# Kernel tuning notes

Hardware: AMD Instinct MI355X
Metric: run time of the kernel (lower is better)

Reference implementation:

```python
import jax, jax.numpy as jnp
import numpy as np

D = 256
H = 256
B = 128
T = 512


def _init_cell(key, input_size, hidden_size):
    K = 1.0 / np.sqrt(hidden_size)
    k1, k2, k3, k4 = jax.random.split(key, 4)
    u = lambda k, shape: jax.random.uniform(k, shape, jnp.float32, -K, K)
    return (u(k1, (3 * hidden_size, input_size)),
            u(k2, (3 * hidden_size, hidden_size)),
            u(k3, (3 * hidden_size,)),
            u(k4, (3 * hidden_size,)))


def setup_inputs() -> dict:
    key = jax.random.key(0)
    kx, kf, kb = jax.random.split(key, 3)
    x = jax.random.normal(kx, (B, T, D), dtype=jnp.float32)
    w_ih_fw, w_hh_fw, b_ih_fw, b_hh_fw = _init_cell(kf, D, H)
    w_ih_bw, w_hh_bw, b_ih_bw, b_hh_bw = _init_cell(kb, D, H)
    return {
        "x": x,
        "w_ih_fw": w_ih_fw, "w_hh_fw": w_hh_fw, "b_ih_fw": b_ih_fw, "b_hh_fw": b_hh_fw,
        "w_ih_bw": w_ih_bw, "w_hh_bw": w_hh_bw, "b_ih_bw": b_ih_bw, "b_hh_bw": b_hh_bw,
    }


def _gru_scan(x_tbd, w_ih, w_hh, b_ih, b_hh):
    # x_tbd: [T, B, D]; returns outputs [T, B, H] and final h [B, H]
    h0 = jnp.zeros((x_tbd.shape[1], H), dtype=x_tbd.dtype)

    def step(h, x_t):
        xT = x_t @ w_ih.T + b_ih          # [B, 3H]
        hT = h @ w_hh.T + b_hh            # [B, 3H]
        s = jax.nn.sigmoid(xT + hT)
        r = s[:, :H]
        z = s[:, H:2 * H]
        n = jnp.tanh(xT[:, 2 * H:] + r * hT[:, 2 * H:])
        h_new = (1.0 - z) * n + z * h
        return h_new, h_new

    h_last, outs = jax.lax.scan(step, h0, x_tbd)
    return outs, h_last


def reference(x, w_ih_fw, w_hh_fw, b_ih_fw, b_hh_fw,
              w_ih_bw, w_hh_bw, b_ih_bw, b_hh_bw):
    x_tbd = jnp.swapaxes(x, 0, 1)                         # [T, B, D]
    outs_fw, h_fw = _gru_scan(x_tbd, w_ih_fw, w_hh_fw, b_ih_fw, b_hh_fw)
    outs_bw_rev, h_bw = _gru_scan(x_tbd[::-1], w_ih_bw, w_hh_bw, b_ih_bw, b_hh_bw)
    outs_bw = outs_bw_rev[::-1]
    outputs = jnp.concatenate([outs_fw, outs_bw], axis=-1)  # [T, B, 2H]
    outputs = jnp.swapaxes(outputs, 0, 1)                   # [B, T, 2H]
    return outputs, h_fw, h_bw
```

## Files before the change

kernel.cpp:

```cpp
#include <hip/hip_runtime.h>
#include <stdint.h>
#include <stddef.h>

#define T_ 512
#define B_ 128
#define D_ 256
#define H_ 256
#define NR 768
#define OUT_MAIN 33554432ull
#define XT_STRIDE 12288
#define HB 280

typedef __attribute__((ext_vector_type(4))) float f32x4;
typedef __attribute__((ext_vector_type(8))) short s16x8;

__device__ __forceinline__ unsigned short f2bf(float f) {
    union { float f; uint32_t u; } v; v.f = f;
    return (unsigned short)((v.u + 0x7FFFu + ((v.u >> 16) & 1u)) >> 16);
}
__device__ __forceinline__ float bf2f(unsigned short h) {
    union { uint32_t u; float f; } v; v.u = ((uint32_t)h) << 16;
    return v.f;
}
__device__ __forceinline__ float sigm(float x) {
    return __builtin_amdgcn_rcpf(1.f + __expf(-x));
}
__device__ __forceinline__ float tanh_(float x) {
    float e = __expf(2.f * x);
    return 1.f - 2.f * __builtin_amdgcn_rcpf(e + 1.f);
}
__device__ __forceinline__ s16x8 pack8(const float* f) {
    union { s16x8 v; unsigned short u[8]; } p;
#pragma unroll
    for (int i = 0; i < 8; ++i) p.u[i] = f2bf(f[i]);
    return p.v;
}

__global__ void k_convert(const float* __restrict__ wf, const float* __restrict__ wb,
                          unsigned short* __restrict__ dst) {
    int i = blockIdx.x * blockDim.x + threadIdx.x;
    const int n = NR * D_;
    if (i < n) dst[i] = f2bf(wf[i]);
    else if (i < 2 * n) dst[i] = f2bf(wb[i - n]);
}

__global__ __launch_bounds__(512, 2) void k_xgemm(
    const float* __restrict__ x, const unsigned short* __restrict__ wbf,
    const float* __restrict__ bih_f, const float* __restrict__ bhh_f,
    const float* __restrict__ bih_b, const float* __restrict__ bhh_b,
    unsigned short* __restrict__ XT)
{
    __shared__ __align__(16) unsigned short lds_a[64 * 72];
    const int tid = threadIdx.x;
    const int lane = tid & 63, wn = tid >> 6;
    const int t = blockIdx.x;
    const int dir = blockIdx.y >> 1, mh = blockIdx.y & 1;

    f32x4 acc[4][6];
#pragma unroll
    for (int m = 0; m < 4; ++m)
#pragma unroll
        for (int n = 0; n < 6; ++n) acc[m][n] = (f32x4){0.f, 0.f, 0.f, 0.f};

    for (int kb = 0; kb < 4; ++kb) {
        if (kb) __syncthreads();
        {
            int row = tid >> 3, seg = tid & 7;
            const float* src = x + ((size_t)(mh * 64 + row) * T_ + t) * D_ + kb * 64 + seg * 8;
            float fv[8];
            *(f32x4*)&fv[0] = *(const f32x4*)(src);
            *(f32x4*)&fv[4] = *(const f32x4*)(src + 4);
            *(s16x8*)&lds_a[row * 72 + seg * 8] = pack8(fv);
        }
        __syncthreads();
#pragma unroll
        for (int kt = 0; kt < 2; ++kt) {
            s16x8 av[4];
#pragma unroll
            for (int mt = 0; mt < 4; ++mt) {
                int r = mt * 16 + (lane & 15);
                av[mt] = *(const s16x8*)&lds_a[r * 72 + kt * 32 + (lane >> 4) * 8];
            }
#pragma unroll
            for (int nt = 0; nt < 6; ++nt) {
                int c = dir * NR + wn * 96 + nt * 16 + (lane & 15);
                s16x8 bv = *(const s16x8*)(wbf + (size_t)c * D_ + kb * 64 + kt * 32 + (lane >> 4) * 8);
#pragma unroll
                for (int mt = 0; mt < 4; ++mt)
                    acc[mt][nt] = __builtin_amdgcn_mfma_f32_16x16x32_bf16(av[mt], bv, acc[mt][nt], 0, 0, 0);
            }
        }
    }
    const float* bih = dir ? bih_b : bih_f;
    const float* bhh = dir ? bhh_b : bhh_f;
#pragma unroll
    for (int nt = 0; nt < 6; ++nt) {
        const int cw = wn * 96 + nt * 16 + (lane & 15);
        const int gate = cw >> 8, j = cw & 255;
        const int jt = (j >> 4) & 1;
        const int rtid = (j >> 5) * 64 + (((lane >> 4)) << 4) + (j & 15);
        float bias = bih[cw] + (cw < 512 ? bhh[cw] : 0.f);
#pragma unroll
        for (int mt = 0; mt < 4; ++mt) {
#pragma unroll
            for (int q = 0; q < 4; ++q) {
                int rr = mh * 64 + mt * 16 + (lane >> 4) * 4 + q;
                int bgrp = rr >> 4;
                int v = (jt * 4 + q) * 3 + gate;
                XT[((size_t)(dir * 8 + bgrp) * T_ + t) * XT_STRIDE + (size_t)rtid * 24 + v]
                    = f2bf(acc[mt][nt][q] + bias);
            }
        }
    }
}

template<int P>
__device__ __forceinline__ void gru_step(
    int s, int dir, int b0, int tid, int lane, int wid,
    const unsigned short* __restrict__ XTw, float* __restrict__ out,
    unsigned short* hb, const s16x8 (&fB)[6][8], float bhn0, float bhn1,
    s16x8 (&CUR)[3], s16x8 (&NXT)[3])
{
    const int t  = dir ? (T_ - 1 - s) : s;
    const int sn = (s < T_ - 1) ? s + 1 : s;
    const int tn = dir ? (T_ - 1 - sn) : sn;
    {
        const s16x8* p = (const s16x8*)(XTw + (size_t)tn * XT_STRIDE) + (size_t)tid * 3;
        NXT[0] = p[0]; NXT[1] = p[1]; NXT[2] = p[2];
    }
    const unsigned short* hr = hb + P * (16 * HB);
    unsigned short*       hw = hb + (P ^ 1) * (16 * HB);

    f32x4 acc[6];
#pragma unroll
    for (int n = 0; n < 6; ++n) acc[n] = (f32x4){0.f, 0.f, 0.f, 0.f};
#pragma unroll
    for (int k0 = 0; k0 < 8; ++k0) {
        s16x8 a = *(const s16x8*)&hr[(lane & 15) * HB + k0 * 32 + (lane >> 4) * 8];
#pragma unroll
        for (int nt = 0; nt < 6; ++nt)
            acc[nt] = __builtin_amdgcn_mfma_f32_16x16x32_bf16(a, fB[nt][k0], acc[nt], 0, 0, 0);
    }
#pragma unroll
    for (int jt = 0; jt < 2; ++jt) {
        const int j = 32 * wid + jt * 16 + (lane & 15);
        const float bn = jt ? bhn1 : bhn0;
#pragma unroll
        for (int q = 0; q < 4; ++q) {
            const int row = (lane >> 4) * 4 + q;
            const int v = (jt * 4 + q) * 3;
            float xr = bf2f((unsigned short)CUR[(v + 0) >> 3][(v + 0) & 7]);
            float xz = bf2f((unsigned short)CUR[(v + 1) >> 3][(v + 1) & 7]);
            float xn = bf2f((unsigned short)CUR[(v + 2) >> 3][(v + 2) & 7]);
            float hv = bf2f(hr[row * HB + j]);
            float rg = sigm(acc[jt][q] + xr);
            float zg = sigm(acc[2 + jt][q] + xz);
            float ng = tanh_(xn + rg * (acc[4 + jt][q] + bn));
            float hnew = ng + zg * (hv - ng);
            hw[row * HB + j] = f2bf(hnew);
            size_t off = ((size_t)(b0 + row) << 18) + ((size_t)t << 9) + (size_t)dir * 256 + j;
            out[off] = hnew;
            if (s == T_ - 1)
                out[OUT_MAIN + (size_t)dir * B_ * H_ + (size_t)(b0 + row) * H_ + j] = hnew;
        }
    }
    __builtin_amdgcn_sched_barrier(0);
    asm volatile("s_waitcnt lgkmcnt(0)");
    __builtin_amdgcn_s_barrier();
    __builtin_amdgcn_sched_barrier(0);
}

__global__ __launch_bounds__(512, 2) void k_recur(
    const float* __restrict__ whh_f, const float* __restrict__ whh_b,
    const float* __restrict__ bhh_f, const float* __restrict__ bhh_b,
    const unsigned short* __restrict__ XT,
    float* __restrict__ out)
{
    __shared__ __align__(16) unsigned short hb[2 * 16 * HB];
    const int tid = threadIdx.x, lane = tid & 63, wid = tid >> 6;
    const int bid = blockIdx.x;
    const int dir = bid >> 3, b0 = (bid & 7) * 16;
    const float* whh = dir ? whh_b : whh_f;
    const float* bhh = dir ? bhh_b : bhh_f;

    s16x8 fB[6][8];
#pragma unroll
    for (int g = 0; g < 3; ++g) {
#pragma unroll
        for (int half = 0; half < 2; ++half) {
            int nt = 2 * g + half;
            int cb = g * 256 + 32 * wid + half * 16;
#pragma unroll
            for (int k0 = 0; k0 < 8; ++k0) {
                const float* sp = whh + (size_t)(cb + (lane & 15)) * H_ + k0 * 32 + (lane >> 4) * 8;
                float fv[8];
                *(f32x4*)&fv[0] = *(const f32x4*)(sp);
                *(f32x4*)&fv[4] = *(const f32x4*)(sp + 4);
                fB[nt][k0] = pack8(fv);
            }
        }
    }
    const float bhn0 = bhh[512 + 32 * wid + (lane & 15)];
    const float bhn1 = bhh[512 + 32 * wid + 16 + (lane & 15)];

    for (int i = tid; i < 16 * HB / 2; i += 512) ((uint32_t*)hb)[i] = 0;
    __syncthreads();

    const unsigned short* XTw = XT + (size_t)(dir * 8 + (bid & 7)) * T_ * XT_STRIDE;
    s16x8 XA[3], XB[3];
    {
        const int t0 = dir ? (T_ - 1) : 0;
        const s16x8* p = (const s16x8*)(XTw + (size_t)t0 * XT_STRIDE) + (size_t)tid * 3;
        XA[0] = p[0]; XA[1] = p[1]; XA[2] = p[2];
    }
#pragma unroll 1
    for (int s = 0; s < T_; s += 2) {
        gru_step<0>(s,     dir, b0, tid, lane, wid, XTw, out, hb, fB, bhn0, bhn1, XA, XB);
        gru_step<1>(s + 1, dir, b0, tid, lane, wid, XTw, out, hb, fB, bhn0, bhn1, XB, XA);
    }
}

extern "C" void kernel_launch(void* const* d_in, const int* in_sizes, int n_in,
                              void* d_out, int out_size, void* d_ws, size_t ws_size,
                              hipStream_t stream) {
    const float* x     = (const float*)d_in[0];
    const float* wih_f = (const float*)d_in[1];
    const float* whh_f = (const float*)d_in[2];
    const float* bih_f = (const float*)d_in[3];
    const float* bhh_f = (const float*)d_in[4];
    const float* wih_b = (const float*)d_in[5];
    const float* whh_b = (const float*)d_in[6];
    const float* bih_b = (const float*)d_in[7];
    const float* bhh_b = (const float*)d_in[8];
    float* out = (float*)d_out;

    unsigned short* wbf = (unsigned short*)d_ws;
    unsigned short* XT  = (unsigned short*)((char*)d_ws + 786432);

    k_convert<<<dim3(768), dim3(512), 0, stream>>>(wih_f, wih_b, wbf);
    k_xgemm<<<dim3(512, 4), dim3(512), 0, stream>>>(x, wbf, bih_f, bhh_f, bih_b, bhh_b, XT);
    k_recur<<<dim3(16), dim3(512), 0, stream>>>(whh_f, whh_b, bhh_f, bhh_b, XT, out);
}
```

Measured before the change: 1.695 ms.

## Keep hidden state in registers and move output stores after the step barrier

The recurrent step now keeps each thread's previous hidden values in fp32 registers instead of re-reading them from LDS. It preloads all eight A fragments before the MFMA chain and uses a hardware pack instruction for bf16 conversion. Global output stores are moved after the barrier so they overlap the next step's work instead of sitting on the critical path. Precision also changes slightly, since the blend now uses the fp32 register value rather than the bf16-rounded LDS copy, and register pressure rises.

```diff
diff --git a/kernel.cpp b/kernel.cpp
--- a/kernel.cpp
+++ b/kernel.cpp
@@ -13,14 +13,22 @@
 
 typedef __attribute__((ext_vector_type(4))) float f32x4;
 typedef __attribute__((ext_vector_type(8))) short s16x8;
+typedef __attribute__((ext_vector_type(4))) uint32_t u32x4;
 
 __device__ __forceinline__ unsigned short f2bf(float f) {
     union { float f; uint32_t u; } v; v.f = f;
     return (unsigned short)((v.u + 0x7FFFu + ((v.u >> 16) & 1u)) >> 16);
 }
-__device__ __forceinline__ float bf2f(unsigned short h) {
-    union { uint32_t u; float f; } v; v.u = ((uint32_t)h) << 16;
-    return v.f;
+__device__ __forceinline__ float lo16(uint32_t w) {
+    union { uint32_t u; float f; } v; v.u = w << 16; return v.f;
+}
+__device__ __forceinline__ float hi16(uint32_t w) {
+    union { uint32_t u; float f; } v; v.u = w & 0xffff0000u; return v.f;
+}
+__device__ __forceinline__ uint32_t cvt1bf(float x) {
+    uint32_t r;
+    asm("v_cvt_pk_bf16_f32 %0, %1, %2" : "=v"(r) : "v"(x), "v"(x));
+    return r;
 }
 __device__ __forceinline__ float sigm(float x) {
     return __builtin_amdgcn_rcpf(1.f + __expf(-x));
@@ -119,55 +127,90 @@
     int s, int dir, int b0, int tid, int lane, int wid,
     const unsigned short* __restrict__ XTw, float* __restrict__ out,
     unsigned short* hb, const s16x8 (&fB)[6][8], float bhn0, float bhn1,
-    s16x8 (&CUR)[3], s16x8 (&NXT)[3])
+    u32x4 (&CUR)[3], u32x4 (&NXT)[3], float (&hreg)[8])
 {
     const int t  = dir ? (T_ - 1 - s) : s;
     const int sn = (s < T_ - 1) ? s + 1 : s;
     const int tn = dir ? (T_ - 1 - sn) : sn;
     {
-        const s16x8* p = (const s16x8*)(XTw + (size_t)tn * XT_STRIDE) + (size_t)tid * 3;
+        const u32x4* p = (const u32x4*)(XTw + (size_t)tn * XT_STRIDE) + (size_t)tid * 3;
         NXT[0] = p[0]; NXT[1] = p[1]; NXT[2] = p[2];
     }
     const unsigned short* hr = hb + P * (16 * HB);
     unsigned short*       hw = hb + (P ^ 1) * (16 * HB);
 
+    s16x8 a[8];
+#pragma unroll
+    for (int k0 = 0; k0 < 8; ++k0)
+        a[k0] = *(const s16x8*)&hr[(lane & 15) * HB + k0 * 32 + (lane >> 4) * 8];
+
     f32x4 acc[6];
 #pragma unroll
     for (int n = 0; n < 6; ++n) acc[n] = (f32x4){0.f, 0.f, 0.f, 0.f};
 #pragma unroll
     for (int k0 = 0; k0 < 8; ++k0) {
-        s16x8 a = *(const s16x8*)&hr[(lane & 15) * HB + k0 * 32 + (lane >> 4) * 8];
 #pragma unroll
         for (int nt = 0; nt < 6; ++nt)
-            acc[nt] = __builtin_amdgcn_mfma_f32_16x16x32_bf16(a, fB[nt][k0], acc[nt], 0, 0, 0);
-    }
+            acc[nt] = __builtin_amdgcn_mfma_f32_16x16x32_bf16(a[k0], fB[nt][k0], acc[nt], 0, 0, 0);
+    }
+
+    float hn[8];
 #pragma unroll
     for (int jt = 0; jt < 2; ++jt) {
-        const int j = 32 * wid + jt * 16 + (lane & 15);
         const float bn = jt ? bhn1 : bhn0;
 #pragma unroll
         for (int q = 0; q < 4; ++q) {
-            const int row = (lane >> 4) * 4 + q;
-            const int v = (jt * 4 + q) * 3;
-            float xr = bf2f((unsigned short)CUR[(v + 0) >> 3][(v + 0) & 7]);
-            float xz = bf2f((unsigned short)CUR[(v + 1) >> 3][(v + 1) & 7]);
-            float xn = bf2f((unsigned short)CUR[(v + 2) >> 3][(v + 2) & 7]);
-            float hv = bf2f(hr[row * HB + j]);
+            const int idx = jt * 4 + q;
+            const int v = idx * 3;
+            uint32_t w0 = CUR[(v)     >> 3][((v)     >> 1) & 3];
+            uint32_t w1 = CUR[(v + 1) >> 3][((v + 1) >> 1) & 3];
+            uint32_t w2 = CUR[(v + 2) >> 3][((v + 2) >> 1) & 3];
+            float xr = (v & 1)       ? hi16(w0) : lo16(w0);
+            float xz = ((v + 1) & 1) ? hi16(w1) : lo16(w1);
+            float xn = ((v + 2) & 1) ? hi16(w2) : lo16(w2);
             float rg = sigm(acc[jt][q] + xr);
             float zg = sigm(acc[2 + jt][q] + xz);
             float ng = tanh_(xn + rg * (acc[4 + jt][q] + bn));
-            float hnew = ng + zg * (hv - ng);
-            hw[row * HB + j] = f2bf(hnew);
-            size_t off = ((size_t)(b0 + row) << 18) + ((size_t)t << 9) + (size_t)dir * 256 + j;
-            out[off] = hnew;
-            if (s == T_ - 1)
-                out[OUT_MAIN + (size_t)dir * B_ * H_ + (size_t)(b0 + row) * H_ + j] = hnew;
+            hn[idx] = ng + zg * (hreg[idx] - ng);
+            hreg[idx] = hn[idx];
+        }
+    }
+#pragma unroll
+    for (int jt = 0; jt < 2; ++jt) {
+        const int j = 32 * wid + jt * 16 + (lane & 15);
+#pragma unroll
+        for (int q = 0; q < 4; ++q) {
+            const int row = (lane >> 4) * 4 + q;
+            hw[row * HB + j] = (unsigned short)cvt1bf(hn[jt * 4 + q]);
         }
     }
     __builtin_amdgcn_sched_barrier(0);
     asm volatile("s_waitcnt lgkmcnt(0)");
     __builtin_amdgcn_s_barrier();
     __builtin_amdgcn_sched_barrier(0);
+
+#pragma unroll
+    for (int jt = 0; jt < 2; ++jt) {
+        const int j = 32 * wid + jt * 16 + (lane & 15);
+#pragma unroll
+        for (int q = 0; q < 4; ++q) {
+            const int row = (lane >> 4) * 4 + q;
+            out[((size_t)(b0 + row) << 18) + ((size_t)t << 9) + (size_t)dir * 256 + j]
+                = hn[jt * 4 + q];
+        }
+    }
+    if (s == T_ - 1) {
+#pragma unroll
+        for (int jt = 0; jt < 2; ++jt) {
+            const int j = 32 * wid + jt * 16 + (lane & 15);
+#pragma unroll
+            for (int q = 0; q < 4; ++q) {
+                const int row = (lane >> 4) * 4 + q;
+                out[OUT_MAIN + (size_t)dir * B_ * H_ + (size_t)(b0 + row) * H_ + j]
+                    = hn[jt * 4 + q];
+            }
+        }
+    }
 }
 
 __global__ __launch_bounds__(512, 2) void k_recur(
@@ -207,16 +250,19 @@
     __syncthreads();
 
     const unsigned short* XTw = XT + (size_t)(dir * 8 + (bid & 7)) * T_ * XT_STRIDE;
-    s16x8 XA[3], XB[3];
+    u32x4 XA[3], XB[3];
+    float hreg[8];
+#pragma unroll
+    for (int i = 0; i < 8; ++i) hreg[i] = 0.f;
     {
         const int t0 = dir ? (T_ - 1) : 0;
-        const s16x8* p = (const s16x8*)(XTw + (size_t)t0 * XT_STRIDE) + (size_t)tid * 3;
+        const u32x4* p = (const u32x4*)(XTw + (size_t)t0 * XT_STRIDE) + (size_t)tid * 3;
         XA[0] = p[0]; XA[1] = p[1]; XA[2] = p[2];
     }
 #pragma unroll 1
     for (int s = 0; s < T_; s += 2) {
-        gru_step<0>(s,     dir, b0, tid, lane, wid, XTw, out, hb, fB, bhn0, bhn1, XA, XB);
-        gru_step<1>(s + 1, dir, b0, tid, lane, wid, XTw, out, hb, fB, bhn0, bhn1, XB, XA);
+        gru_step<0>(s,     dir, b0, tid, lane, wid, XTw, out, hb, fB, bhn0, bhn1, XA, XB, hreg);
+        gru_step<1>(s + 1, dir, b0, tid, lane, wid, XTw, out, hb, fB, bhn0, bhn1, XB, XA, hreg);
     }
 }
 
```

Result: slower. 2.562 ms (+51.2%).

## Stage xgemm output in LDS for coalesced XT stores, halve M per block

Applied to the files above, without the earlier changes.

The input-projection GEMM kernel now writes its bf16 results into a shared-memory tile laid out in XT order, then copies it to global memory with 16-byte vector stores instead of scattered 2-byte stores. Each block now covers 32 batch rows instead of 64, doubling the grid, and input conversion uses the hardware packed bf16 convert instruction. The recurrent kernel's XT indexing is simplified to match. This costs more LDS and extra barriers per block, and B-fragment reuse per block is lower.

```diff
diff --git a/kernel.cpp b/kernel.cpp
--- a/kernel.cpp
+++ b/kernel.cpp
@@ -13,6 +13,8 @@
 
 typedef __attribute__((ext_vector_type(4))) float f32x4;
 typedef __attribute__((ext_vector_type(8))) short s16x8;
+typedef __attribute__((ext_vector_type(4))) uint32_t u32x4;
+typedef __attribute__((ext_vector_type(2))) uint32_t u32x2;
 
 __device__ __forceinline__ unsigned short f2bf(float f) {
     union { float f; uint32_t u; } v; v.f = f;
@@ -21,6 +23,11 @@
 __device__ __forceinline__ float bf2f(unsigned short h) {
     union { uint32_t u; float f; } v; v.u = ((uint32_t)h) << 16;
     return v.f;
+}
+__device__ __forceinline__ uint32_t cvtpk(float a, float b) {
+    uint32_t r;
+    asm("v_cvt_pk_bf16_f32 %0, %1, %2" : "=v"(r) : "v"(a), "v"(b));
+    return r;
 }
 __device__ __forceinline__ float sigm(float x) {
     return __builtin_amdgcn_rcpf(1.f + __expf(-x));
@@ -50,34 +57,33 @@
     const float* __restrict__ bih_b, const float* __restrict__ bhh_b,
     unsigned short* __restrict__ XT)
 {
-    __shared__ __align__(16) unsigned short lds_a[64 * 72];
-    const int tid = threadIdx.x;
-    const int lane = tid & 63, wn = tid >> 6;
+    __shared__ __align__(16) unsigned short lds_a[32 * 72];
+    __shared__ __align__(16) unsigned short xt_l[2 * XT_STRIDE];
+    const int tid = threadIdx.x, lane = tid & 63, wn = tid >> 6;
     const int t = blockIdx.x;
-    const int dir = blockIdx.y >> 1, mh = blockIdx.y & 1;
-
-    f32x4 acc[4][6];
-#pragma unroll
-    for (int m = 0; m < 4; ++m)
+    const int dir = blockIdx.y >> 2, q2 = blockIdx.y & 3;
+
+    f32x4 acc[2][6];
+#pragma unroll
+    for (int m = 0; m < 2; ++m)
 #pragma unroll
         for (int n = 0; n < 6; ++n) acc[m][n] = (f32x4){0.f, 0.f, 0.f, 0.f};
 
     for (int kb = 0; kb < 4; ++kb) {
         if (kb) __syncthreads();
         {
-            int row = tid >> 3, seg = tid & 7;
-            const float* src = x + ((size_t)(mh * 64 + row) * T_ + t) * D_ + kb * 64 + seg * 8;
-            float fv[8];
-            *(f32x4*)&fv[0] = *(const f32x4*)(src);
-            *(f32x4*)&fv[4] = *(const f32x4*)(src + 4);
-            *(s16x8*)&lds_a[row * 72 + seg * 8] = pack8(fv);
+            int row = tid >> 4, c4 = (tid & 15) * 4;
+            const float* src = x + ((size_t)(q2 * 32 + row) * T_ + t) * D_ + kb * 64 + c4;
+            f32x4 f = *(const f32x4*)src;
+            u32x2 p = { cvtpk(f[0], f[1]), cvtpk(f[2], f[3]) };
+            *(u32x2*)&lds_a[row * 72 + c4] = p;
         }
         __syncthreads();
 #pragma unroll
         for (int kt = 0; kt < 2; ++kt) {
-            s16x8 av[4];
-#pragma unroll
-            for (int mt = 0; mt < 4; ++mt) {
+            s16x8 av[2];
+#pragma unroll
+            for (int mt = 0; mt < 2; ++mt) {
                 int r = mt * 16 + (lane & 15);
                 av[mt] = *(const s16x8*)&lds_a[r * 72 + kt * 32 + (lane >> 4) * 8];
             }
@@ -86,31 +92,38 @@
                 int c = dir * NR + wn * 96 + nt * 16 + (lane & 15);
                 s16x8 bv = *(const s16x8*)(wbf + (size_t)c * D_ + kb * 64 + kt * 32 + (lane >> 4) * 8);
 #pragma unroll
-                for (int mt = 0; mt < 4; ++mt)
+                for (int mt = 0; mt < 2; ++mt)
                     acc[mt][nt] = __builtin_amdgcn_mfma_f32_16x16x32_bf16(av[mt], bv, acc[mt][nt], 0, 0, 0);
             }
         }
     }
     const float* bih = dir ? bih_b : bih_f;
     const float* bhh = dir ? bhh_b : bhh_f;
+    __syncthreads();
 #pragma unroll
     for (int nt = 0; nt < 6; ++nt) {
         const int cw = wn * 96 + nt * 16 + (lane & 15);
         const int gate = cw >> 8, j = cw & 255;
         const int jt = (j >> 4) & 1;
-        const int rtid = (j >> 5) * 64 + (((lane >> 4)) << 4) + (j & 15);
+        const int rtid = (j >> 5) * 64 + ((lane >> 4) << 4) + (j & 15);
         float bias = bih[cw] + (cw < 512 ? bhh[cw] : 0.f);
 #pragma unroll
-        for (int mt = 0; mt < 4; ++mt) {
+        for (int mt = 0; mt < 2; ++mt) {
 #pragma unroll
             for (int q = 0; q < 4; ++q) {
-                int rr = mh * 64 + mt * 16 + (lane >> 4) * 4 + q;
-                int bgrp = rr >> 4;
                 int v = (jt * 4 + q) * 3 + gate;
-                XT[((size_t)(dir * 8 + bgrp) * T_ + t) * XT_STRIDE + (size_t)rtid * 24 + v]
-                    = f2bf(acc[mt][nt][q] + bias);
-            }
-        }
+                xt_l[mt * XT_STRIDE + rtid * 24 + v] = f2bf(acc[mt][nt][q] + bias);
+            }
+        }
+    }
+    __syncthreads();
+#pragma unroll
+    for (int half = 0; half < 2; ++half) {
+        size_t base = ((size_t)(dir * 8 + q2 * 2 + half) * T_ + t) * XT_STRIDE;
+#pragma unroll
+        for (int k = 0; k < 3; ++k)
+            *(u32x4*)(XT + base + (size_t)tid * 24 + k * 8)
+                = *(const u32x4*)&xt_l[half * XT_STRIDE + tid * 24 + k * 8];
     }
 }
 
@@ -206,7 +219,7 @@
     for (int i = tid; i < 16 * HB / 2; i += 512) ((uint32_t*)hb)[i] = 0;
     __syncthreads();
 
-    const unsigned short* XTw = XT + (size_t)(dir * 8 + (bid & 7)) * T_ * XT_STRIDE;
+    const unsigned short* XTw = XT + (size_t)bid * T_ * XT_STRIDE;
     s16x8 XA[3], XB[3];
     {
         const int t0 = dir ? (T_ - 1) : 0;
@@ -238,6 +251,6 @@
     unsigned short* XT  = (unsigned short*)((char*)d_ws + 786432);
 
     k_convert<<<dim3(768), dim3(512), 0, stream>>>(wih_f, wih_b, wbf);
-    k_xgemm<<<dim3(512, 4), dim3(512), 0, stream>>>(x, wbf, bih_f, bhh_f, bih_b, bhh_b, XT);
+    k_xgemm<<<dim3(512, 8), dim3(512), 0, stream>>>(x, wbf, bih_f, bhh_f, bih_b, bhh_b, XT);
     k_recur<<<dim3(16), dim3(512), 0, stream>>>(whh_f, whh_b, bhh_f, bhh_b, XT, out);
 }
```

Measured after the change: 1.467 ms, median of 2. 13.5% less time.
